# Kernel optimization log

Measured on AMD Instinct MI355X. Metric: run time of the kernel, lower is better.

Reference implementation:

```python
import jax, jax.numpy as jnp
import numpy as np

B, N, IN_C, OUT_C, HID, H = 4, 2048, 3, 1, 256, 8
V = HID // H  # v_dim per head
LOCALITIES = (50, 30, 60, 80)  # down=loc[0], PA0=loc[0], PA1=loc[1], up=loc[-1] (as in torch code)


def _gelu(x):
    return jax.nn.gelu(x, approximate=False)  # torch F.gelu default is exact erf


def _pos_att(m_dist, x, r, w, locality):
    # m_dist: [N,N], x: [B,N,HID], r: [H,1,1], w: [H,HID,V]
    scale = jnp.tan(0.25 * np.pi * (1.0 - 1e-7) * (1.0 + jnp.sin(r)))  # [H,1,1]
    sd = m_dist[None, :, :] * scale  # [H,N,N]
    if locality <= 100:
        thr = jnp.quantile(sd, locality / 100.0, axis=-1, keepdims=True)  # [H,N,1]
        sd = jnp.where(sd <= thr, sd, jnp.inf)
    att = jax.nn.softmax(-sd, axis=-1)  # masked entries -> 0
    value = jnp.einsum('bnj,hjk->bhnk', x, w)   # [B,H,N,V]
    out = jnp.einsum('hjn,bhnk->bhjk', att, value)  # [B,H,N,V]
    b, j = out.shape[0], out.shape[2]
    out = out.transpose(0, 2, 1, 3).reshape(b, j, -1)  # [B,N,HID]
    return _gelu(out)


def setup_inputs() -> dict:
    key = jax.random.key(0)
    ks = jax.random.split(key, 32)
    rn = lambda i, shape: jax.random.normal(ks[i], shape, dtype=jnp.float32)
    s = 0.02
    z = lambda d: jnp.zeros((d,), dtype=jnp.float32)
    return {
        'x': rn(0, (B, N, IN_C)),
        'm_dist0': jax.random.uniform(ks[1], (N, N), dtype=jnp.float32),
        'm_dist1': jax.random.uniform(ks[2], (N, N), dtype=jnp.float32),
        'm_dist2': jax.random.uniform(ks[3], (N, N), dtype=jnp.float32),
        'm_dist3': jax.random.uniform(ks[4], (N, N), dtype=jnp.float32),
        'en_w': rn(5, (IN_C, HID)) * s, 'en_b': z(HID),
        'down_r': rn(6, (H, 1, 1)), 'down_w': rn(7, (H, HID, V)) * s,
        'pa0_r': rn(8, (H, 1, 1)), 'pa0_w': rn(9, (H, HID, V)) * s,
        'pa1_r': rn(10, (H, 1, 1)), 'pa1_w': rn(11, (H, HID, V)) * s,
        'mlp0_w1': rn(12, (HID, HID)) * s, 'mlp0_b1': z(HID),
        'mlp0_w2': rn(13, (HID, HID)) * s, 'mlp0_b2': z(HID),
        'w0_w': rn(14, (HID, HID)) * s, 'w0_b': z(HID),
        'mlp1_w1': rn(15, (HID, HID)) * s, 'mlp1_b1': z(HID),
        'mlp1_w2': rn(16, (HID, HID)) * s, 'mlp1_b2': z(HID),
        'w1_w': rn(17, (HID, HID)) * s, 'w1_b': z(HID),
        'up_r': rn(18, (H, 1, 1)), 'up_w': rn(19, (H, HID, V)) * s,
        'de1_w': rn(20, (HID, HID)) * s, 'de1_b': z(HID),
        'de2_w': rn(21, (HID, OUT_C)) * s, 'de2_b': z(OUT_C),
    }


def reference(x, m_dist0, m_dist1, m_dist2, m_dist3, en_w, en_b,
              down_r, down_w, pa0_r, pa0_w, pa1_r, pa1_w,
              mlp0_w1, mlp0_b1, mlp0_w2, mlp0_b2, w0_w, w0_b,
              mlp1_w1, mlp1_b1, mlp1_w2, mlp1_b2, w1_w, w1_b,
              up_r, up_w, de1_w, de1_b, de2_w, de2_b):
    h = _gelu(x @ en_w + en_b)
    h = _pos_att(m_dist0, h, down_r, down_w, LOCALITIES[0])
    # block 0 (PA[0] uses localities[0], m_dists[1])
    a = _pos_att(m_dist1, h, pa0_r, pa0_w, LOCALITIES[0])
    h = _gelu((_gelu(a @ mlp0_w1 + mlp0_b1) @ mlp0_w2 + mlp0_b2) + (h @ w0_w + w0_b))
    # block 1 (PA[1] uses localities[1], m_dists[2])
    a = _pos_att(m_dist2, h, pa1_r, pa1_w, LOCALITIES[1])
    h = _gelu((_gelu(a @ mlp1_w1 + mlp1_b1) @ mlp1_w2 + mlp1_b2) + (h @ w1_w + w1_b))
    h = _pos_att(m_dist3, h, up_r, up_w, LOCALITIES[3])
    h = _gelu(h @ de1_w + de1_b)
    return h @ de2_w + de2_b
```

## Files before the change

kernel.cpp:

```cpp
#include <hip/hip_runtime.h>

#define NB 4
#define NN 2048
#define HIDDEN 256
#define NH 8
#define VD 32

typedef float f4 __attribute__((ext_vector_type(4)));

__device__ __forceinline__ float gelu_f(float v) {
    return 0.5f * v * (1.0f + erff(v * 0.7071067811865475f));
}

__global__ void k_encode(const float* __restrict__ x, const float* __restrict__ w,
                         const float* __restrict__ b, float* __restrict__ out) {
    int id = blockIdx.x * 256 + threadIdx.x;
    int c = id & 255, rn = id >> 8;
    float acc = b[c];
    acc += x[rn * 3 + 0] * w[c] + x[rn * 3 + 1] * w[256 + c] + x[rn * 3 + 2] * w[512 + c];
    out[id] = gelu_f(acc);
}

__global__ __launch_bounds__(256) void k_thrsel(const float* __restrict__ m,
        const float* __restrict__ rv, float* __restrict__ thr,
        float* __restrict__ mmin, float* __restrict__ invD, int kcount)
{
    __shared__ float rowf[NN];
    __shared__ unsigned hist[256];
    __shared__ float redf[32];
    __shared__ unsigned redu[4];
    __shared__ unsigned s_bin, s_below;
    const int row = blockIdx.x, t = threadIdx.x;
    const int lane = t & 63, wid = t >> 6;
    const float* mr = m + (size_t)row * NN;

    float lmin = 3.4e38f;
    for (int i = t; i < NN; i += 256) { float v = mr[i]; rowf[i] = v; lmin = fminf(lmin, v); }
#pragma unroll
    for (int d = 32; d > 0; d >>= 1) lmin = fminf(lmin, __shfl_xor(lmin, d, 64));
    if (lane == 0) redf[wid] = lmin;
    __syncthreads();
    const float rmin = fminf(fminf(redf[0], redf[1]), fminf(redf[2], redf[3]));

    unsigned prefix = 0; int want = kcount;
    const unsigned hmasks[4] = {0u, 0xFF000000u, 0xFFFF0000u, 0xFFFFFF00u};
    for (int pass = 0; pass < 4; ++pass) {
        const int shift = 24 - 8 * pass;
        hist[t] = 0;
        __syncthreads();
        const unsigned hm = hmasks[pass];
        for (int i = t; i < NN; i += 256) {
            unsigned u = __float_as_uint(rowf[i]);
            u ^= (u & 0x80000000u) ? 0xFFFFFFFFu : 0x80000000u;
            if ((u & hm) == (prefix & hm))
                atomicAdd(&hist[(u >> shift) & 255u], 1u);
        }
        __syncthreads();
        const unsigned cnt = hist[t];
        unsigned v = cnt;
#pragma unroll
        for (int d = 1; d < 64; d <<= 1) {
            unsigned o = __shfl_up(v, d, 64);
            if (lane >= d) v += o;
        }
        if (lane == 63) redu[wid] = v;
        __syncthreads();
        unsigned woff = 0;
#pragma unroll
        for (int w = 0; w < 3; w++) if (w < wid) woff += redu[w];
        const unsigned incl = v + woff;
        const unsigned below = incl - cnt;
        if (incl >= (unsigned)want && below < (unsigned)want) { s_bin = (unsigned)t; s_below = below; }
        __syncthreads();
        want -= (int)s_below;
        prefix |= (s_bin << shift);
    }
    unsigned ku = prefix;
    ku = (ku & 0x80000000u) ? (ku & 0x7FFFFFFFu) : ~ku;
    const float tf = __uint_as_float(ku);

    const float cc = (float)(0.25 * 3.141592653589793 * (1.0 - 1e-7));
    float sch[NH], lacc[NH];
#pragma unroll
    for (int h = 0; h < NH; h++) { sch[h] = tanf(cc * (1.0f + sinf(rv[h]))); lacc[h] = 0.f; }
    for (int i = t; i < NN; i += 256) {
        float v = rowf[i];
        if (v <= tf) {
            float d = v - rmin;
#pragma unroll
            for (int h = 0; h < NH; h++) lacc[h] += expf(-sch[h] * d);
        }
    }
#pragma unroll
    for (int h = 0; h < NH; h++) {
#pragma unroll
        for (int d = 32; d > 0; d >>= 1) lacc[h] += __shfl_xor(lacc[h], d, 64);
    }
    if (lane == 0) {
#pragma unroll
        for (int h = 0; h < NH; h++) redf[wid * 8 + h] = lacc[h];
    }
    __syncthreads();
    if (t < NH)
        invD[t * NN + row] = 1.0f / (redf[t] + redf[8 + t] + redf[16 + t] + redf[24 + t]);
    if (t == 0) { thr[row] = tf; mmin[row] = rmin; }
}

__global__ __launch_bounds__(256) void k_gemm(const float* __restrict__ A,
        const float* __restrict__ Wm, const float* __restrict__ bias,
        const float* __restrict__ addsrc, float* __restrict__ Cm, int act, int wmode)
{
    __shared__ float AsT[64 * 68];
    __shared__ float Ws[64 * 68];
    const int r0 = blockIdx.x * 64;
    const int c0 = blockIdx.y * 64;
    const int t = threadIdx.x;
    const int ty = t >> 4, tx = t & 15;
    float acc[4][4] = {};
    for (int k0 = 0; k0 < 256; k0 += 64) {
        __syncthreads();
#pragma unroll
        for (int l = 0; l < 16; l++) {
            int lin = l * 256 + t;
            int rr = lin >> 6, kk = lin & 63;
            AsT[kk * 68 + rr] = A[(size_t)(r0 + rr) * 256 + k0 + kk];
            Ws[rr * 68 + kk] = wmode
                ? Wm[(size_t)((c0 + kk) >> 5) * (HIDDEN * VD) + (size_t)(k0 + rr) * VD + ((c0 + kk) & 31)]
                : Wm[(size_t)(k0 + rr) * 256 + c0 + kk];
        }
        __syncthreads();
#pragma unroll 8
        for (int kk = 0; kk < 64; kk++) {
            const float4 a4 = *(const float4*)&AsT[kk * 68 + ty * 4];
            const float4 w4 = *(const float4*)&Ws[kk * 68 + tx * 4];
            float av[4] = {a4.x, a4.y, a4.z, a4.w};
            float wv[4] = {w4.x, w4.y, w4.z, w4.w};
#pragma unroll
            for (int q = 0; q < 4; q++)
#pragma unroll
                for (int p = 0; p < 4; p++)
                    acc[q][p] = fmaf(av[q], wv[p], acc[q][p]);
        }
    }
#pragma unroll
    for (int q = 0; q < 4; q++) {
        int r = r0 + ty * 4 + q;
#pragma unroll
        for (int p = 0; p < 4; p++) {
            int c = c0 + tx * 4 + p;
            float v = acc[q][p];
            if (bias) v += bias[c];
            if (addsrc) v += addsrc[(size_t)r * 256 + c];
            if (act) v = gelu_f(v);
            Cm[(size_t)r * 256 + c] = v;
        }
    }
}

template<int WMODE>
__global__ __launch_bounds__(256) void k_gemm9(const float* __restrict__ A,
        const float* __restrict__ Wm, float* __restrict__ G0, float* __restrict__ G1)
{
    __shared__ float AsT[64 * 68];
    __shared__ float Ws[64 * 68];
    const int r0 = blockIdx.x * 64;
    const int c0 = blockIdx.y * 64;
    const int kbase = blockIdx.z * 128;
    float* __restrict__ G = blockIdx.z ? G1 : G0;
    const int t = threadIdx.x;
    const int ty = t >> 4, tx = t & 15;
    float acc[4][4] = {};
    for (int kh = 0; kh < 128; kh += 64) {
        const int k0 = kbase + kh;
        __syncthreads();
#pragma unroll
        for (int l = 0; l < 16; l++) {
            int lin = l * 256 + t;
            int rr = lin >> 6, kk = lin & 63;
            AsT[kk * 68 + rr] = A[(size_t)(r0 + rr) * 256 + k0 + kk];
            Ws[rr * 68 + kk] = WMODE
                ? Wm[(size_t)((c0 + kk) >> 5) * (HIDDEN * VD) + (size_t)(k0 + rr) * VD + ((c0 + kk) & 31)]
                : Wm[(size_t)(k0 + rr) * 256 + c0 + kk];
        }
        __syncthreads();
#pragma unroll 8
        for (int kk = 0; kk < 64; kk++) {
            const float4 a4 = *(const float4*)&AsT[kk * 68 + ty * 4];
            const float4 w4 = *(const float4*)&Ws[kk * 68 + tx * 4];
            float av[4] = {a4.x, a4.y, a4.z, a4.w};
            float wv[4] = {w4.x, w4.y, w4.z, w4.w};
#pragma unroll
            for (int q = 0; q < 4; q++)
#pragma unroll
                for (int p = 0; p < 4; p++)
                    acc[q][p] = fmaf(av[q], wv[p], acc[q][p]);
        }
    }
#pragma unroll
    for (int q = 0; q < 4; q++) {
        const int r = r0 + ty * 4 + q;
        f4 st;
#pragma unroll
        for (int p = 0; p < 4; p++) st[p] = acc[q][p];
        *(f4*)&G[(size_t)r * 256 + c0 + tx * 4] = st;
    }
}

__global__ __launch_bounds__(256) void k_gemmcomb(const float* __restrict__ g0,
        const float* __restrict__ g1, const float* __restrict__ bias,
        const float* __restrict__ addsrc, float* __restrict__ out, int act)
{
    int gid = blockIdx.x * 256 + threadIdx.x;
    int idx = gid * 4;
    int c = idx & 255;
    f4 a = *(const f4*)&g0[idx];
    f4 b = *(const f4*)&g1[idx];
    f4 s;
#pragma unroll
    for (int k = 0; k < 4; k++) s[k] = a[k] + b[k];
    if (bias) {
        f4 bb = *(const f4*)&bias[c];
#pragma unroll
        for (int k = 0; k < 4; k++) s[k] += bb[k];
    }
    if (addsrc) {
        f4 r = *(const f4*)&addsrc[idx];
#pragma unroll
        for (int k = 0; k < 4; k++) s[k] += r[k];
    }
    if (act) {
#pragma unroll
        for (int k = 0; k < 4; k++) s[k] = gelu_f(s[k]);
    }
    *(f4*)&out[idx] = s;
}

#define TJA 32
__global__ __launch_bounds__(256, 2) void k_attapply6(
    const float* __restrict__ m, const float* __restrict__ v2,
    const float* __restrict__ rv, const float* __restrict__ thr,
    const float* __restrict__ mmin,
    float* __restrict__ P0, float* __restrict__ P1,
    float* __restrict__ P2, float* __restrict__ P3, int jlen)
{
    __shared__ float Es[128 * 36];
    __shared__ float Vs[TJA * 132];
    const int head = blockIdx.x >> 4;
    const int i0 = (blockIdx.x & 15) * 128;
    const int jbase = blockIdx.y * jlen;
    float* __restrict__ P = (blockIdx.y == 0) ? P0 : (blockIdx.y == 1) ? P1
                          : (blockIdx.y == 2) ? P2 : P3;
    const int t = threadIdx.x;
    const int tx = t & 15, ty = t >> 4;
    const int txm = t & 7, tym = t >> 3;
    const int c4 = t & 31, jw = t >> 5;
    const int bbv = c4 >> 3, kkv = (c4 & 7) * 4;
    const float cc = (float)(0.25 * 3.141592653589793 * (1.0 - 1e-7));
    const float scale = tanf(cc * (1.0f + sinf(rv[head])));

    float thr_r[4], mmn_r[4];
#pragma unroll
    for (int q = 0; q < 4; q++) {
        thr_r[q] = thr[i0 + q * 32 + tym];
        mmn_r[q] = mmin[i0 + q * 32 + tym];
    }

    float acc[8][8];
#pragma unroll
    for (int q = 0; q < 8; q++)
#pragma unroll
        for (int p = 0; p < 8; p++) acc[q][p] = 0.f;

    f4 pm[4], pv[4];
    const int NT = jlen / TJA;

#define A_LOAD(S)                                                              \
    do {                                                                       \
        const int j0 = jbase + (S) * TJA;                                      \
        _Pragma("unroll")                                                      \
        for (int q = 0; q < 4; q++)                                            \
            pm[q] = *(const f4*)&m[(size_t)(i0 + q * 32 + tym) * NN + j0 + 4 * txm]; \
        _Pragma("unroll")                                                      \
        for (int l = 0; l < 4; l++)                                            \
            pv[l] = *(const f4*)&v2[(((size_t)bbv * NN) + j0 + l * 8 + jw) * HIDDEN + head * VD + kkv]; \
    } while (0)

#define A_STORE()                                                              \
    do {                                                                       \
        _Pragma("unroll")                                                      \
        for (int q = 0; q < 4; q++) {                                          \
            f4 ev;                                                             \
            _Pragma("unroll")                                                  \
            for (int d = 0; d < 4; d++) {                                      \
                float e = 0.f;                                                 \
                if (pm[q][d] <= thr_r[q]) e = expf(-scale * (pm[q][d] - mmn_r[q])); \
                ev[d] = e;                                                     \
            }                                                                  \
            *(f4*)&Es[(q * 32 + tym) * 36 + 4 * txm] = ev;                     \
        }                                                                      \
        _Pragma("unroll")                                                      \
        for (int l = 0; l < 4; l++)                                            \
            *(f4*)&Vs[(l * 8 + jw) * 132 + 4 * c4] = pv[l];                    \
    } while (0)

    A_LOAD(0);
    A_STORE();
    __syncthreads();

    for (int s = 0; s < NT; s++) {
        if (s + 1 < NT) A_LOAD(s + 1);
        for (int jc = 0; jc < TJA; jc += 4) {
            f4 ev[8], va[4], vb[4];
#pragma unroll
            for (int q = 0; q < 8; q++)
                ev[q] = *(const f4*)&Es[(q * 16 + ty) * 36 + jc];
#pragma unroll
            for (int d = 0; d < 4; d++) {
                va[d] = *(const f4*)&Vs[(jc + d) * 132 + 4 * tx];
                vb[d] = *(const f4*)&Vs[(jc + d) * 132 + 64 + 4 * tx];
            }
#pragma unroll
            for (int d = 0; d < 4; d++) {
#pragma unroll
                for (int q = 0; q < 8; q++) {
                    const float e = ev[q][d];
#pragma unroll
                    for (int p = 0; p < 4; p++) {
                        acc[q][p]     = fmaf(e, va[d][p], acc[q][p]);
                        acc[q][p + 4] = fmaf(e, vb[d][p], acc[q][p + 4]);
                    }
                }
            }
        }
        if (s + 1 < NT) {
            __syncthreads();
            A_STORE();
            __syncthreads();
        }
    }
#undef A_LOAD
#undef A_STORE

    const int bba = tx >> 3, kka = (tx & 7) * 4;
#pragma unroll
    for (int q = 0; q < 8; q++) {
        const int gi = i0 + q * 16 + ty;
        f4 sa, sb;
#pragma unroll
        for (int p = 0; p < 4; p++) { sa[p] = acc[q][p]; sb[p] = acc[q][p + 4]; }
        *(f4*)&P[(((size_t)bba * NN) + gi) * HIDDEN + head * VD + kka] = sa;
        *(f4*)&P[(((size_t)(bba + 2) * NN) + gi) * HIDDEN + head * VD + kka] = sb;
    }
}

__global__ __launch_bounds__(256) void k_attcombine(const float* __restrict__ p1,
        const float* __restrict__ p2, const float* __restrict__ p3,
        const float* __restrict__ invD, float* __restrict__ io)
{
    int gid = blockIdx.x * 256 + threadIdx.x;
    int idx = gid * 4;
    int hid = idx & (HIDDEN - 1);
    int i = (idx >> 8) & (NN - 1);
    float sD = invD[(hid >> 5) * NN + i];
    f4 a = *(const f4*)&io[idx];
    f4 b = *(const f4*)&p1[idx];
    f4 s;
#pragma unroll
    for (int k = 0; k < 4; k++) s[k] = a[k] + b[k];
    if (p2) {
        f4 c = *(const f4*)&p2[idx];
        f4 d = *(const f4*)&p3[idx];
#pragma unroll
        for (int k = 0; k < 4; k++) s[k] += c[k] + d[k];
    }
#pragma unroll
    for (int k = 0; k < 4; k++) s[k] = gelu_f(s[k] * sD);
    *(f4*)&io[idx] = s;
}

__global__ void k_decode(const float* __restrict__ a, const float* __restrict__ w,
                         const float* __restrict__ b, float* __restrict__ out) {
    int gid = blockIdx.x * 256 + threadIdx.x;
    int row = gid >> 6, lane = threadIdx.x & 63;
    const float* ar = a + (size_t)row * HIDDEN;
    float s = ar[lane] * w[lane] + ar[lane + 64] * w[lane + 64]
            + ar[lane + 128] * w[lane + 128] + ar[lane + 192] * w[lane + 192];
    for (int off = 32; off > 0; off >>= 1) s += __shfl_down(s, off);
    if (lane == 0) out[row] = s + b[0];
}

extern "C" void kernel_launch(void* const* d_in, const int* in_sizes, int n_in,
                              void* d_out, int out_size, void* d_ws, size_t ws_size,
                              hipStream_t stream)
{
    (void)in_sizes; (void)n_in; (void)out_size;
    const float* x      = (const float*)d_in[0];
    const float* m0     = (const float*)d_in[1];
    const float* m1     = (const float*)d_in[2];
    const float* m2     = (const float*)d_in[3];
    const float* m3     = (const float*)d_in[4];
    const float* en_w   = (const float*)d_in[5];
    const float* en_b   = (const float*)d_in[6];
    const float* down_r = (const float*)d_in[7];
    const float* down_w = (const float*)d_in[8];
    const float* pa0_r  = (const float*)d_in[9];
    const float* pa0_w  = (const float*)d_in[10];
    const float* pa1_r  = (const float*)d_in[11];
    const float* pa1_w  = (const float*)d_in[12];
    const float* mlp0_w1= (const float*)d_in[13];
    const float* mlp0_b1= (const float*)d_in[14];
    const float* mlp0_w2= (const float*)d_in[15];
    const float* mlp0_b2= (const float*)d_in[16];
    const float* w0_w   = (const float*)d_in[17];
    const float* w0_b   = (const float*)d_in[18];
    const float* mlp1_w1= (const float*)d_in[19];
    const float* mlp1_b1= (const float*)d_in[20];
    const float* mlp1_w2= (const float*)d_in[21];
    const float* mlp1_b2= (const float*)d_in[22];
    const float* w1_w   = (const float*)d_in[23];
    const float* w1_b   = (const float*)d_in[24];
    const float* up_r   = (const float*)d_in[25];
    const float* up_w   = (const float*)d_in[26];
    const float* de1_w  = (const float*)d_in[27];
    const float* de1_b  = (const float*)d_in[28];
    const float* de2_w  = (const float*)d_in[29];
    const float* de2_b  = (const float*)d_in[30];
    float* out = (float*)d_out;

    float* WS = (float*)d_ws;
    const size_t SZ = (size_t)NB * NN * HIDDEN;
    float* Hb  = WS;
    float* Ab  = Hb + SZ;
    float* Vb  = Ab + SZ;
    float* T1  = Vb + SZ;
    float* THR = T1 + SZ;
    float* MMIN= THR + NN;
    float* INVD= MMIN + NN;
    float* P2  = INVD + NH * NN;
    float* P3  = P2 + SZ;
    const size_t need4 = (size_t)((P3 + SZ) - WS) * sizeof(float);
    const int JS = (ws_size >= need4) ? 4 : 2;
    float* T3  = Vb;

    auto gemm = [&](const float* A, const float* W, const float* bias,
                    const float* add, float* dst, int act, int wmode) {
        if (JS == 4) {
            if (wmode)
                hipLaunchKernelGGL((k_gemm9<1>), dim3(128, 4, 2), dim3(256), 0, stream,
                                   A, W, P2, P3);
            else
                hipLaunchKernelGGL((k_gemm9<0>), dim3(128, 4, 2), dim3(256), 0, stream,
                                   A, W, P2, P3);
            hipLaunchKernelGGL(k_gemmcomb, dim3((int)(SZ / 4 / 256)), dim3(256), 0, stream,
                               P2, P3, bias, add, dst, act);
        } else {
            hipLaunchKernelGGL(k_gemm, dim3(128, 4), dim3(256), 0, stream,
                               A, W, bias, add, dst, act, wmode);
        }
    };

    auto posatt = [&](const float* src, float* dst2, const float* md,
                      const float* r, const float* w, int kc) {
        hipLaunchKernelGGL(k_thrsel, dim3(NN), dim3(256), 0, stream, md, r, THR, MMIN, INVD, kc);
        gemm(src, w, nullptr, nullptr, Vb, 0, 1);
        hipLaunchKernelGGL(k_attapply6, dim3(128, JS), dim3(256), 0, stream,
                           md, Vb, r, THR, MMIN, dst2, T1, P2, P3, NN / JS);
        hipLaunchKernelGGL(k_attcombine, dim3((int)(SZ / 4 / 256)), dim3(256), 0, stream,
                           T1, (JS == 4) ? P2 : (const float*)nullptr,
                           (JS == 4) ? P3 : (const float*)nullptr, INVD, dst2);
    };

    float* curH = Hb; float* oth = Ab;
    hipLaunchKernelGGL(k_encode, dim3(8192), dim3(256), 0, stream, x, en_w, en_b, curH);

    posatt(curH, oth, m0, down_r, down_w, 1024);
    { float* tmp = curH; curH = oth; oth = tmp; }

    posatt(curH, oth, m1, pa0_r, pa0_w, 1024);
    gemm(curH, w0_w, w0_b, nullptr, T3, 0, 0);
    gemm(oth, mlp0_w1, mlp0_b1, nullptr, T1, 1, 0);
    gemm(T1, mlp0_w2, mlp0_b2, T3, oth, 1, 0);
    { float* tmp = curH; curH = oth; oth = tmp; }

    posatt(curH, oth, m2, pa1_r, pa1_w, 615);
    gemm(curH, w1_w, w1_b, nullptr, T3, 0, 0);
    gemm(oth, mlp1_w1, mlp1_b1, nullptr, T1, 1, 0);
    gemm(T1, mlp1_w2, mlp1_b2, T3, oth, 1, 0);
    { float* tmp = curH; curH = oth; oth = tmp; }

    posatt(curH, oth, m3, up_r, up_w, 1638);
    { float* tmp = curH; curH = oth; oth = tmp; }

    gemm(curH, de1_w, de1_b, nullptr, T1, 1, 0);
    hipLaunchKernelGGL(k_decode, dim3(2048), dim3(256), 0, stream, T1, de2_w, de2_b, out);
}
```

Baseline: 872.5 us.

## Batch all four threshold selections into one launch and double-buffer attention tiles

The four per-layer quantile/threshold kernels become a single launch over a 2D grid (row x layer), with results written to per-layer slices of the workspace. This removes three launches and gives the GPU more independent blocks at once. The attention-apply kernel now ping-pongs between two shared-memory tile buffers, so the next tile is stored while the current one is being computed and one barrier per tile is saved. The cost is double the LDS per block, which may limit occupancy below the two blocks requested by the launch bounds, and a slightly larger workspace.

```diff
diff --git a/kernel.cpp b/kernel.cpp
--- a/kernel.cpp
+++ b/kernel.cpp
@@ -21,9 +21,13 @@
     out[id] = gelu_f(acc);
 }
 
-__global__ __launch_bounds__(256) void k_thrsel(const float* __restrict__ m,
-        const float* __restrict__ rv, float* __restrict__ thr,
-        float* __restrict__ mmin, float* __restrict__ invD, int kcount)
+__global__ __launch_bounds__(256) void k_thrsel4(
+        const float* __restrict__ m0, const float* __restrict__ m1,
+        const float* __restrict__ m2, const float* __restrict__ m3,
+        const float* __restrict__ r0, const float* __restrict__ r1,
+        const float* __restrict__ r2, const float* __restrict__ r3,
+        int k0, int k1, int k2, int k3,
+        float* __restrict__ thr, float* __restrict__ mmin, float* __restrict__ invD)
 {
     __shared__ float rowf[NN];
     __shared__ unsigned hist[256];
@@ -31,8 +35,12 @@
     __shared__ unsigned redu[4];
     __shared__ unsigned s_bin, s_below;
     const int row = blockIdx.x, t = threadIdx.x;
+    const int c = blockIdx.y;
     const int lane = t & 63, wid = t >> 6;
-    const float* mr = m + (size_t)row * NN;
+    const float* mb = (c == 0) ? m0 : (c == 1) ? m1 : (c == 2) ? m2 : m3;
+    const float* rv = (c == 0) ? r0 : (c == 1) ? r1 : (c == 2) ? r2 : r3;
+    const int kcount = (c == 0) ? k0 : (c == 1) ? k1 : (c == 2) ? k2 : k3;
+    const float* mr = mb + (size_t)row * NN;
 
     float lmin = 3.4e38f;
     for (int i = t; i < NN; i += 256) { float v = mr[i]; rowf[i] = v; lmin = fminf(lmin, v); }
@@ -102,8 +110,8 @@
     }
     __syncthreads();
     if (t < NH)
-        invD[t * NN + row] = 1.0f / (redf[t] + redf[8 + t] + redf[16 + t] + redf[24 + t]);
-    if (t == 0) { thr[row] = tf; mmin[row] = rmin; }
+        invD[(c * NH + t) * NN + row] = 1.0f / (redf[t] + redf[8 + t] + redf[16 + t] + redf[24 + t]);
+    if (t == 0) { thr[c * NN + row] = tf; mmin[c * NN + row] = rmin; }
 }
 
 __global__ __launch_bounds__(256) void k_gemm(const float* __restrict__ A,
@@ -236,20 +244,22 @@
 }
 
 #define TJA 32
-__global__ __launch_bounds__(256, 2) void k_attapply6(
+__global__ __launch_bounds__(256, 2) void k_attapply8(
     const float* __restrict__ m, const float* __restrict__ v2,
     const float* __restrict__ rv, const float* __restrict__ thr,
     const float* __restrict__ mmin,
     float* __restrict__ P0, float* __restrict__ P1,
     float* __restrict__ P2, float* __restrict__ P3, int jlen)
 {
-    __shared__ float Es[128 * 36];
-    __shared__ float Vs[TJA * 132];
+    __shared__ float EsA[128 * 36];
+    __shared__ float VsA[TJA * 132];
+    __shared__ float EsB[128 * 36];
+    __shared__ float VsB[TJA * 132];
     const int head = blockIdx.x >> 4;
     const int i0 = (blockIdx.x & 15) * 128;
     const int jbase = blockIdx.y * jlen;
-    float* __restrict__ P = (blockIdx.y == 0) ? P0 : (blockIdx.y == 1) ? P1
-                          : (blockIdx.y == 2) ? P2 : P3;
+    const int by = blockIdx.y;
+    float* __restrict__ P = (by == 0) ? P0 : (by == 1) ? P1 : (by == 2) ? P2 : P3;
     const int t = threadIdx.x;
     const int tx = t & 15, ty = t >> 4;
     const int txm = t & 7, tym = t >> 3;
@@ -285,7 +295,7 @@
             pv[l] = *(const f4*)&v2[(((size_t)bbv * NN) + j0 + l * 8 + jw) * HIDDEN + head * VD + kkv]; \
     } while (0)
 
-#define A_STORE()                                                              \
+#define A_STORE(ES, VS)                                                        \
     do {                                                                       \
         _Pragma("unroll")                                                      \
         for (int q = 0; q < 4; q++) {                                          \
@@ -296,50 +306,61 @@
                 if (pm[q][d] <= thr_r[q]) e = expf(-scale * (pm[q][d] - mmn_r[q])); \
                 ev[d] = e;                                                     \
             }                                                                  \
-            *(f4*)&Es[(q * 32 + tym) * 36 + 4 * txm] = ev;                     \
+            *(f4*)&ES[(q * 32 + tym) * 36 + 4 * txm] = ev;                     \
         }                                                                      \
         _Pragma("unroll")                                                      \
         for (int l = 0; l < 4; l++)                                            \
-            *(f4*)&Vs[(l * 8 + jw) * 132 + 4 * c4] = pv[l];                    \
+            *(f4*)&VS[(l * 8 + jw) * 132 + 4 * c4] = pv[l];                    \
     } while (0)
 
+#define A_COMPUTE(ES, VS)                                                      \
+    do {                                                                       \
+        for (int jc = 0; jc < TJA; jc += 4) {                                  \
+            f4 ev[8], va[4], vb[4];                                            \
+            _Pragma("unroll")                                                  \
+            for (int q = 0; q < 8; q++)                                        \
+                ev[q] = *(const f4*)&ES[(q * 16 + ty) * 36 + jc];              \
+            _Pragma("unroll")                                                  \
+            for (int d = 0; d < 4; d++) {                                      \
+                va[d] = *(const f4*)&VS[(jc + d) * 132 + 4 * tx];              \
+                vb[d] = *(const f4*)&VS[(jc + d) * 132 + 64 + 4 * tx];         \
+            }                                                                  \
+            _Pragma("unroll")                                                  \
+            for (int d = 0; d < 4; d++) {                                      \
+                _Pragma("unroll")                                              \
+                for (int q = 0; q < 8; q++) {                                  \
+                    const float e = ev[q][d];                                  \
+                    _Pragma("unroll")                                          \
+                    for (int p = 0; p < 4; p++) {                              \
+                        acc[q][p]     = fmaf(e, va[d][p], acc[q][p]);          \
+                        acc[q][p + 4] = fmaf(e, vb[d][p], acc[q][p + 4]);      \
+                    }                                                          \
+                }                                                              \
+            }                                                                  \
+        }                                                                      \
+    } while (0)
+
     A_LOAD(0);
-    A_STORE();
+    A_STORE(EsA, VsA);
     __syncthreads();
 
-    for (int s = 0; s < NT; s++) {
+    for (int s = 0; s < NT; s += 2) {
         if (s + 1 < NT) A_LOAD(s + 1);
-        for (int jc = 0; jc < TJA; jc += 4) {
-            f4 ev[8], va[4], vb[4];
-#pragma unroll
-            for (int q = 0; q < 8; q++)
-                ev[q] = *(const f4*)&Es[(q * 16 + ty) * 36 + jc];
-#pragma unroll
-            for (int d = 0; d < 4; d++) {
-                va[d] = *(const f4*)&Vs[(jc + d) * 132 + 4 * tx];
-                vb[d] = *(const f4*)&Vs[(jc + d) * 132 + 64 + 4 * tx];
-            }
-#pragma unroll
-            for (int d = 0; d < 4; d++) {
-#pragma unroll
-                for (int q = 0; q < 8; q++) {
-                    const float e = ev[q][d];
-#pragma unroll
-                    for (int p = 0; p < 4; p++) {
-                        acc[q][p]     = fmaf(e, va[d][p], acc[q][p]);
-                        acc[q][p + 4] = fmaf(e, vb[d][p], acc[q][p + 4]);
-                    }
-                }
-            }
-        }
+        A_COMPUTE(EsA, VsA);
         if (s + 1 < NT) {
+            A_STORE(EsB, VsB);
             __syncthreads();
-            A_STORE();
+        }
+        if (s + 2 < NT) A_LOAD(s + 2);
+        if (s + 1 < NT) A_COMPUTE(EsB, VsB);
+        if (s + 2 < NT) {
+            A_STORE(EsA, VsA);
             __syncthreads();
         }
     }
 #undef A_LOAD
 #undef A_STORE
+#undef A_COMPUTE
 
     const int bba = tx >> 3, kka = (tx & 7) * 4;
 #pragma unroll
@@ -429,22 +450,22 @@
 
     float* WS = (float*)d_ws;
     const size_t SZ = (size_t)NB * NN * HIDDEN;
-    float* Hb  = WS;
-    float* Ab  = Hb + SZ;
-    float* Vb  = Ab + SZ;
-    float* T1  = Vb + SZ;
-    float* THR = T1 + SZ;
-    float* MMIN= THR + NN;
-    float* INVD= MMIN + NN;
-    float* P2  = INVD + NH * NN;
-    float* P3  = P2 + SZ;
+    float* Hb   = WS;
+    float* Ab   = Hb + SZ;
+    float* Vb   = Ab + SZ;
+    float* T1   = Vb + SZ;
+    float* THR4 = T1 + SZ;
+    float* MMIN4= THR4 + 4 * NN;
+    float* INVD4= MMIN4 + 4 * NN;
+    float* P2   = INVD4 + 4 * NH * NN;
+    float* P3   = P2 + SZ;
     const size_t need4 = (size_t)((P3 + SZ) - WS) * sizeof(float);
     const int JS = (ws_size >= need4) ? 4 : 2;
-    float* T3  = Vb;
+    float* T3   = Vb;
 
     auto gemm = [&](const float* A, const float* W, const float* bias,
                     const float* add, float* dst, int act, int wmode) {
-        if (JS == 4) {
+        if (JS >= 4) {
             if (wmode)
                 hipLaunchKernelGGL((k_gemm9<1>), dim3(128, 4, 2), dim3(256), 0, stream,
                                    A, W, P2, P3);
@@ -459,36 +480,41 @@
         }
     };
 
-    auto posatt = [&](const float* src, float* dst2, const float* md,
-                      const float* r, const float* w, int kc) {
-        hipLaunchKernelGGL(k_thrsel, dim3(NN), dim3(256), 0, stream, md, r, THR, MMIN, INVD, kc);
+    hipLaunchKernelGGL(k_thrsel4, dim3(NN, 4), dim3(256), 0, stream,
+                       m0, m1, m2, m3, down_r, pa0_r, pa1_r, up_r,
+                       1024, 1024, 615, 1638, THR4, MMIN4, INVD4);
+
+    auto posatt = [&](int c, const float* src, float* dst2, const float* md,
+                      const float* r, const float* w) {
         gemm(src, w, nullptr, nullptr, Vb, 0, 1);
-        hipLaunchKernelGGL(k_attapply6, dim3(128, JS), dim3(256), 0, stream,
-                           md, Vb, r, THR, MMIN, dst2, T1, P2, P3, NN / JS);
+        hipLaunchKernelGGL(k_attapply8, dim3(128, JS), dim3(256), 0, stream,
+                           md, Vb, r, THR4 + c * NN, MMIN4 + c * NN,
+                           dst2, T1, P2, P3, NN / JS);
         hipLaunchKernelGGL(k_attcombine, dim3((int)(SZ / 4 / 256)), dim3(256), 0, stream,
-                           T1, (JS == 4) ? P2 : (const float*)nullptr,
-                           (JS == 4) ? P3 : (const float*)nullptr, INVD, dst2);
+                           T1, (JS >= 4) ? P2 : (const float*)nullptr,
+                           (JS >= 4) ? P3 : (const float*)nullptr,
+                           INVD4 + c * NH * NN, dst2);
     };
 
     float* curH = Hb; float* oth = Ab;
     hipLaunchKernelGGL(k_encode, dim3(8192), dim3(256), 0, stream, x, en_w, en_b, curH);
 
-    posatt(curH, oth, m0, down_r, down_w, 1024);
+    posatt(0, curH, oth, m0, down_r, down_w);
     { float* tmp = curH; curH = oth; oth = tmp; }
 
-    posatt(curH, oth, m1, pa0_r, pa0_w, 1024);
+    posatt(1, curH, oth, m1, pa0_r, pa0_w);
     gemm(curH, w0_w, w0_b, nullptr, T3, 0, 0);
     gemm(oth, mlp0_w1, mlp0_b1, nullptr, T1, 1, 0);
     gemm(T1, mlp0_w2, mlp0_b2, T3, oth, 1, 0);
     { float* tmp = curH; curH = oth; oth = tmp; }
 
-    posatt(curH, oth, m2, pa1_r, pa1_w, 615);
+    posatt(2, curH, oth, m2, pa1_r, pa1_w);
     gemm(curH, w1_w, w1_b, nullptr, T3, 0, 0);
     gemm(oth, mlp1_w1, mlp1_b1, nullptr, T1, 1, 0);
     gemm(T1, mlp1_w2, mlp1_b2, T3, oth, 1, 0);
     { float* tmp = curH; curH = oth; oth = tmp; }
 
-    posatt(curH, oth, m3, up_r, up_w, 1638);
+    posatt(3, curH, oth, m3, up_r, up_w);
     { float* tmp = curH; curH = oth; oth = tmp; }
 
     gemm(curH, de1_w, de1_b, nullptr, T1, 1, 0);
```

Measured after the change: 844.6 us, median of 2. 3.2% less time.
